# Kernel optimization log

Measured on AMD Instinct MI355X. Metric: run time of the kernel, lower is better.

## Reference

```python
import jax, jax.numpy as jnp
import numpy as np

DIM = 1024
NUM_HEADS = 16
HEAD_DIM = DIM // NUM_HEADS
EPS_NORM = 1e-12  # F.normalize eps
EPS_LN = 1e-5     # nn.LayerNorm eps


def setup_inputs() -> dict:
    key = jax.random.key(0)
    ks = jax.random.split(key, 6)
    x = jax.random.normal(ks[0], (4, 2048, DIM), dtype=jnp.float32)
    # LayerNorm params
    ln_w = jnp.ones((DIM,), jnp.float32)
    ln_b = jnp.zeros((DIM,), jnp.float32)
    # qkv: xavier_uniform on weight [3D, D], zero bias
    limit = float(np.sqrt(6.0 / (DIM + 3 * DIM)))
    qkv_w = jax.random.uniform(ks[1], (3 * DIM, DIM), jnp.float32, -limit, limit)
    qkv_b = jnp.zeros((3 * DIM,), jnp.float32)
    # out_proj: normal std=0.02, zero bias
    out_w = 0.02 * jax.random.normal(ks[2], (DIM, DIM), dtype=jnp.float32)
    out_b = jnp.zeros((DIM,), jnp.float32)
    return {"x": x, "ln_w": ln_w, "ln_b": ln_b, "qkv_w": qkv_w,
            "qkv_b": qkv_b, "out_w": out_w, "out_b": out_b}


def reference(x, ln_w, ln_b, qkv_w, qkv_b, out_w, out_b):
    B, N, D = x.shape
    # pre-LayerNorm
    mu = jnp.mean(x, axis=-1, keepdims=True)
    var = jnp.mean(jnp.square(x - mu), axis=-1, keepdims=True)
    h = (x - mu) / jnp.sqrt(var + EPS_LN) * ln_w + ln_b
    # QKV projection (torch Linear: y = h @ W^T + b)
    qkv = h @ qkv_w.T + qkv_b                     # [B, N, 3D]
    qkv = qkv.reshape(B, N, 3, NUM_HEADS, HEAD_DIM)
    q, k, v = (jnp.transpose(qkv[:, :, i], (0, 2, 1, 3)) for i in range(3))  # [B,H,N,hd]
    # per-head L2 normalize (F.normalize semantics: x / max(||x||, eps))
    q = q / jnp.maximum(jnp.linalg.norm(q, axis=-1, keepdims=True), EPS_NORM)
    k = k / jnp.maximum(jnp.linalg.norm(k, axis=-1, keepdims=True), EPS_NORM)
    scale = HEAD_DIM ** 0.5
    attn = jnp.einsum('bhqd,bhkd->bhqk', q, k) * scale
    attn = jax.nn.softmax(attn, axis=-1)
    out = jnp.einsum('bhqk,bhkd->bhqd', attn, v)  # [B,H,N,hd]
    out = jnp.transpose(out, (0, 2, 1, 3)).reshape(B, N, D)
    return x + out @ out_w.T + out_b
```

## Files before the change

### kernel.cpp

```cpp
#include <hip/hip_runtime.h>
#include <math.h>

constexpr int D     = 1024;
constexpr int NH    = 16;
constexpr int HD    = 64;
constexpr int SEQ   = 2048;
constexpr int BATCH = 4;
constexpr int NTOK  = BATCH * SEQ;

typedef short s16x8 __attribute__((ext_vector_type(8)));
typedef short s16x4 __attribute__((ext_vector_type(4)));
typedef float f32x4 __attribute__((ext_vector_type(4)));
typedef unsigned short u16;
typedef unsigned int   u32;

#if __has_builtin(__builtin_amdgcn_exp2f)
#define EXP2(x) __builtin_amdgcn_exp2f(x)
#else
#define EXP2(x) exp2f(x)
#endif

__device__ __forceinline__ short f2bf(float f) {
    unsigned u = __float_as_uint(f);
    unsigned r = (u + 0x7FFFu + ((u >> 16) & 1u)) >> 16;
    return (short)r;
}
__device__ __forceinline__ float bf2f(u16 s) {
    return __uint_as_float(((unsigned)s) << 16);
}

__device__ __forceinline__ u32 pack_bf16_pair(float f0, float f1) {
    u32 a = __float_as_uint(f1) + 0x8000u;
    u32 b = __float_as_uint(f0) + 0x8000u;
    return __builtin_amdgcn_perm(a, b, 0x07060302u);
}

__device__ __forceinline__ void async_lds16(const void* g, void* l) {
    __builtin_amdgcn_global_load_lds(
        (const __attribute__((address_space(1))) unsigned int*)g,
        (__attribute__((address_space(3))) unsigned int*)l, 16, 0, 0);
}

__device__ __forceinline__ float block_reduce_sum(float v, float* red) {
    int lane = threadIdx.x & 63, wid = threadIdx.x >> 6;
    #pragma unroll
    for (int off = 32; off > 0; off >>= 1) v += __shfl_down(v, off, 64);
    if (lane == 0) red[wid] = v;
    __syncthreads();
    float r = red[0] + red[1] + red[2] + red[3];
    __syncthreads();
    return r;
}

__global__ __launch_bounds__(256) void ln_kernel(const float* __restrict__ x,
                                                 const float* __restrict__ w,
                                                 const float* __restrict__ b,
                                                 u16* __restrict__ h) {
    __shared__ float red[4];
    int row = blockIdx.x;
    const float* xr = x + (size_t)row * D;
    int t = threadIdx.x;
    float v[4];
    float s = 0.f;
    #pragma unroll
    for (int i = 0; i < 4; i++) { v[i] = xr[t + 256 * i]; s += v[i]; }
    float mean = block_reduce_sum(s, red) * (1.0f / 1024.0f);
    float ss = 0.f;
    #pragma unroll
    for (int i = 0; i < 4; i++) { float d = v[i] - mean; ss += d * d; }
    float var = block_reduce_sum(ss, red) * (1.0f / 1024.0f);
    float rstd = rsqrtf(var + 1e-5f);
    u16* hr = h + (size_t)row * D;
    #pragma unroll
    for (int i = 0; i < 4; i++) {
        int c = t + 256 * i;
        hr[c] = (u16)f2bf((v[i] - mean) * rstd * w[c] + b[c]);
    }
}

__global__ __launch_bounds__(256) void cast_kernel(const float* __restrict__ in,
                                                   u16* __restrict__ out, int n) {
    int i = (blockIdx.x * 256 + threadIdx.x) * 4;
    if (i >= n) return;
    float4 f = *(const float4*)(in + i);
    s16x4 o4;
    o4[0] = f2bf(f.x); o4[1] = f2bf(f.y); o4[2] = f2bf(f.z); o4[3] = f2bf(f.w);
    *(s16x4*)(out + i) = o4;
}

template <typename OutT, bool RES, bool NORMK>
__global__ __launch_bounds__(256) void gemm_bf16(const u16* __restrict__ A,
                                                 const u16* __restrict__ B,
                                                 const float* __restrict__ bias,
                                                 const float* __restrict__ R,
                                                 OutT* __restrict__ C,
                                                 int M, int N, int K) {
    __shared__ u16 As[128 * 32];
    __shared__ u16 Bs[128 * 32];
    int tid = threadIdx.x, wave = tid >> 6, lane = tid & 63;
    int quad = lane >> 4, l16 = lane & 15;
    int wm = (wave & 1) * 64, wn = (wave >> 1) * 64;
    int rowBase = blockIdx.y * 128, colBase = blockIdx.x * 128;

    int srow = lane >> 2;
    int sk8  = (lane & 3) * 8;

    f32x4 acc[4][4];
    #pragma unroll
    for (int i = 0; i < 4; i++)
        #pragma unroll
        for (int j = 0; j < 4; j++)
            acc[i][j] = (f32x4){0.f, 0.f, 0.f, 0.f};

    for (int k0 = 0; k0 < K; k0 += 32) {
        __syncthreads();
        #pragma unroll
        for (int i = 0; i < 2; i++) {
            int r = wave * 32 + i * 16;
            const u16* ga = A + (size_t)(rowBase + r + srow) * K + k0 + sk8;
            async_lds16(ga, &As[r * 32]);
            const u16* gb = B + (size_t)(colBase + r + srow) * K + k0 + sk8;
            async_lds16(gb, &Bs[r * 32]);
        }
        __syncthreads();

        s16x8 af[4], bfr[4];
        #pragma unroll
        for (int t = 0; t < 4; t++) {
            af[t]  = *(const s16x8*)&As[(wm + t * 16 + l16) * 32 + quad * 8];
            bfr[t] = *(const s16x8*)&Bs[(wn + t * 16 + l16) * 32 + quad * 8];
        }
        #pragma unroll
        for (int mt = 0; mt < 4; mt++)
            #pragma unroll
            for (int nt = 0; nt < 4; nt++)
                acc[mt][nt] = __builtin_amdgcn_mfma_f32_16x16x32_bf16(
                    af[mt], bfr[nt], acc[mt][nt], 0, 0, 0);
    }

    bool normk = NORMK && (colBase + wn) >= 1024 && (colBase + wn) < 2048;

    #pragma unroll
    for (int mt = 0; mt < 4; mt++) {
        float vals[4][4];
        #pragma unroll
        for (int nt = 0; nt < 4; nt++) {
            int gn = colBase + wn + nt * 16 + l16;
            float bv = bias[gn];
            #pragma unroll
            for (int r = 0; r < 4; r++) {
                float val = acc[mt][nt][r] + bv;
                if (RES) {
                    int gm = rowBase + wm + mt * 16 + quad * 4 + r;
                    val += R[(size_t)gm * N + gn];
                }
                vals[nt][r] = val;
            }
        }
        if (normk) {
            #pragma unroll
            for (int r = 0; r < 4; r++) {
                float ssq = 0.f;
                #pragma unroll
                for (int nt = 0; nt < 4; nt++) ssq = fmaf(vals[nt][r], vals[nt][r], ssq);
                ssq += __shfl_xor(ssq, 1, 64);
                ssq += __shfl_xor(ssq, 2, 64);
                ssq += __shfl_xor(ssq, 4, 64);
                ssq += __shfl_xor(ssq, 8, 64);
                float inv = 1.0f / fmaxf(sqrtf(ssq), 1e-12f);
                #pragma unroll
                for (int nt = 0; nt < 4; nt++) vals[nt][r] *= inv;
            }
        }
        #pragma unroll
        for (int nt = 0; nt < 4; nt++) {
            int gn = colBase + wn + nt * 16 + l16;
            int gm0 = rowBase + wm + mt * 16 + quad * 4;
            #pragma unroll
            for (int r = 0; r < 4; r++) {
                if constexpr (sizeof(OutT) == 2)
                    C[(size_t)(gm0 + r) * N + gn] = (OutT)f2bf(vals[nt][r]);
                else
                    C[(size_t)(gm0 + r) * N + gn] = vals[nt][r];
            }
        }
    }
}

__device__ __forceinline__ s16x8 rdfrag(const u16* lds, int row, int kk, int quad) {
    int byte = row * 128 + ((kk * 64 + quad * 16) ^ ((row & 7) << 4));
    return *(const s16x8*)((const char*)lds + byte);
}

__device__ __forceinline__ void stage_half_A(const u16* __restrict__ A, u16* ldsA,
                                             int rowBase, int K, int kt, int hs,
                                             int wave, int lane) {
    #pragma unroll
    for (int i = 0; i < 2; i++) {
        int c = wave * 2 + i;
        int baserow = ((c & 7) * 8) + ((c >> 3) << 7) + (hs << 6);
        int row = baserow + (lane >> 3);
        int colb = ((lane & 7) * 16) ^ ((row & 7) << 4);
        const u16* src = A + (size_t)(rowBase + row) * K + kt * 64 + (colb >> 1);
        async_lds16(src, ldsA + baserow * 64);
    }
}
__device__ __forceinline__ void stage_half_B(const u16* __restrict__ B, u16* ldsB,
                                             int colBase, int K, int kt, int hs,
                                             int wave, int lane) {
    #pragma unroll
    for (int i = 0; i < 2; i++) {
        int c = wave * 2 + i;
        int baserow = ((c & 3) * 8) + ((c >> 2) << 6) + (hs << 5);
        int row = baserow + (lane >> 3);
        int colb = ((lane & 7) * 16) ^ ((row & 7) << 4);
        const u16* src = B + (size_t)(colBase + row) * K + kt * 64 + (colb >> 1);
        async_lds16(src, ldsB + baserow * 64);
    }
}

template <typename OutT, bool RES, bool NORMK>
__global__ __launch_bounds__(512, 2) void gemm256(const u16* __restrict__ A,
                                                  const u16* __restrict__ B,
                                                  const float* __restrict__ bias,
                                                  const float* __restrict__ R,
                                                  OutT* __restrict__ C,
                                                  int M, int N, int K) {
    __shared__ u16 lds[2][2][256 * 64];

    int nby = M >> 8;
    int cpx = gridDim.x >> 3;
    int bid = blockIdx.x;
    int swz = (bid & 7) * cpx + (bid >> 3);
    int bx = swz / nby, by = swz % nby;
    int rowBase = by << 8, colBase = bx << 8;

    int tid = threadIdx.x, wave = tid >> 6, lane = tid & 63;
    int quad = lane >> 4, l16 = lane & 15;
    int wr = wave >> 2, wc = wave & 3;
    int KT = K >> 6;

    f32x4 acc[8][4];
    #pragma unroll
    for (int m = 0; m < 8; m++)
        #pragma unroll
        for (int n = 0; n < 4; n++)
            acc[m][n] = (f32x4){0.f, 0.f, 0.f, 0.f};

    stage_half_A(A, &lds[0][0][0], rowBase, K, 0, 0, wave, lane);
    stage_half_B(B, &lds[0][1][0], colBase, K, 0, 0, wave, lane);
    stage_half_A(A, &lds[0][0][0], rowBase, K, 0, 1, wave, lane);
    stage_half_B(B, &lds[0][1][0], colBase, K, 0, 1, wave, lane);
    stage_half_A(A, &lds[1][0][0], rowBase, K, 1, 0, wave, lane);
    stage_half_B(B, &lds[1][1][0], colBase, K, 1, 0, wave, lane);
    stage_half_A(A, &lds[1][0][0], rowBase, K, 1, 1, wave, lane);
    asm volatile("s_waitcnt vmcnt(6)" ::: "memory");
    __builtin_amdgcn_s_barrier();

    for (int t = 0; t < KT; ++t) {
        int bsel = t & 1;
        u16* cA = &lds[bsel][0][0];
        u16* cB = &lds[bsel][1][0];
        u16* oB = &lds[bsel ^ 1][1][0];
        int t1 = t + 1; if (t1 >= KT) t1 -= KT;
        int t2 = t + 2; if (t2 >= KT) t2 -= KT;

        s16x8 af[4][2], bf0[2][2], bf1[2][2];

        #pragma unroll
        for (int m = 0; m < 4; m++)
            #pragma unroll
            for (int kk = 0; kk < 2; kk++)
                af[m][kk] = rdfrag(cA, wr * 128 + m * 16 + l16, kk, quad);
        #pragma unroll
        for (int n = 0; n < 2; n++)
            #pragma unroll
            for (int kk = 0; kk < 2; kk++)
                bf0[n][kk] = rdfrag(cB, wc * 64 + n * 16 + l16, kk, quad);
        stage_half_B(B, oB, colBase, K, t1, 1, wave, lane);
        __builtin_amdgcn_s_barrier();
        __builtin_amdgcn_s_setprio(1);
        #pragma unroll
        for (int kk = 0; kk < 2; kk++)
            #pragma unroll
            for (int m = 0; m < 4; m++)
                #pragma unroll
                for (int n = 0; n < 2; n++)
                    acc[m][n] = __builtin_amdgcn_mfma_f32_16x16x32_bf16(
                        af[m][kk], bf0[n][kk], acc[m][n], 0, 0, 0);
        __builtin_amdgcn_s_setprio(0);
        __builtin_amdgcn_s_barrier();

        #pragma unroll
        for (int n = 0; n < 2; n++)
            #pragma unroll
            for (int kk = 0; kk < 2; kk++)
                bf1[n][kk] = rdfrag(cB, wc * 64 + (n + 2) * 16 + l16, kk, quad);
        stage_half_A(A, cA, rowBase, K, t2, 0, wave, lane);
        __builtin_amdgcn_s_barrier();
        __builtin_amdgcn_s_setprio(1);
        #pragma unroll
        for (int kk = 0; kk < 2; kk++)
            #pragma unroll
            for (int m = 0; m < 4; m++)
                #pragma unroll
                for (int n = 0; n < 2; n++)
                    acc[m][n + 2] = __builtin_amdgcn_mfma_f32_16x16x32_bf16(
                        af[m][kk], bf1[n][kk], acc[m][n + 2], 0, 0, 0);
        __builtin_amdgcn_s_setprio(0);
        __builtin_amdgcn_s_barrier();

        #pragma unroll
        for (int m = 0; m < 4; m++)
            #pragma unroll
            for (int kk = 0; kk < 2; kk++)
                af[m][kk] = rdfrag(cA, wr * 128 + (m + 4) * 16 + l16, kk, quad);
        stage_half_B(B, cB, colBase, K, t2, 0, wave, lane);
        __builtin_amdgcn_s_barrier();
        __builtin_amdgcn_s_setprio(1);
        #pragma unroll
        for (int kk = 0; kk < 2; kk++)
            #pragma unroll
            for (int m = 0; m < 4; m++)
                #pragma unroll
                for (int n = 0; n < 2; n++)
                    acc[m + 4][n] = __builtin_amdgcn_mfma_f32_16x16x32_bf16(
                        af[m][kk], bf0[n][kk], acc[m + 4][n], 0, 0, 0);
        __builtin_amdgcn_s_setprio(0);
        __builtin_amdgcn_s_barrier();

        stage_half_A(A, cA, rowBase, K, t2, 1, wave, lane);
        __builtin_amdgcn_s_barrier();
        __builtin_amdgcn_s_setprio(1);
        #pragma unroll
        for (int kk = 0; kk < 2; kk++)
            #pragma unroll
            for (int m = 0; m < 4; m++)
                #pragma unroll
                for (int n = 0; n < 2; n++)
                    acc[m + 4][n + 2] = __builtin_amdgcn_mfma_f32_16x16x32_bf16(
                        af[m][kk], bf1[n][kk], acc[m + 4][n + 2], 0, 0, 0);
        __builtin_amdgcn_s_setprio(0);
        asm volatile("s_waitcnt vmcnt(6)" ::: "memory");
        __builtin_amdgcn_s_barrier();
    }
    asm volatile("s_waitcnt vmcnt(0)" ::: "memory");

    bool normk = NORMK && (colBase + wc * 64) >= 1024 && (colBase + wc * 64) < 2048;

    #pragma unroll
    for (int m = 0; m < 8; m++) {
        float vals[4][4];
        #pragma unroll
        for (int n = 0; n < 4; n++) {
            int gn = colBase + wc * 64 + n * 16 + l16;
            float bv = bias[gn];
            #pragma unroll
            for (int r = 0; r < 4; r++) {
                float val = acc[m][n][r] + bv;
                if (RES) {
                    int gm = rowBase + wr * 128 + m * 16 + quad * 4 + r;
                    val += R[(size_t)gm * N + gn];
                }
                vals[n][r] = val;
            }
        }
        if (normk) {
            #pragma unroll
            for (int r = 0; r < 4; r++) {
                float ssq = 0.f;
                #pragma unroll
                for (int n = 0; n < 4; n++) ssq = fmaf(vals[n][r], vals[n][r], ssq);
                ssq += __shfl_xor(ssq, 1, 64);
                ssq += __shfl_xor(ssq, 2, 64);
                ssq += __shfl_xor(ssq, 4, 64);
                ssq += __shfl_xor(ssq, 8, 64);
                float inv = 1.0f / fmaxf(sqrtf(ssq), 1e-12f);
                #pragma unroll
                for (int n = 0; n < 4; n++) vals[n][r] *= inv;
            }
        }
        #pragma unroll
        for (int n = 0; n < 4; n++) {
            int gn = colBase + wc * 64 + n * 16 + l16;
            int gm0 = rowBase + wr * 128 + m * 16 + quad * 4;
            #pragma unroll
            for (int r = 0; r < 4; r++) {
                if constexpr (sizeof(OutT) == 2)
                    C[(size_t)(gm0 + r) * N + gn] = (OutT)f2bf(vals[n][r]);
                else
                    C[(size_t)(gm0 + r) * N + gn] = vals[n][r];
            }
        }
    }
}

__global__ __launch_bounds__(256, 2) void mha_kernel(const u16* __restrict__ qkv,
                                                     u16* __restrict__ out) {
    __shared__ u16 Ks[64 * 64];
    constexpr int VS = 68;
    __shared__ u16 Vt[64 * VS];

    int bh = blockIdx.x & 63;
    int qt = blockIdx.x >> 6;
    int b  = bh >> 4, h = bh & 15;
    int tid = threadIdx.x;
    int wave = tid >> 6, lane = tid & 63;
    int quad = lane >> 4, l16 = lane & 15;

    const size_t rs = 3072;
    constexpr float SCL = 11.5415605f;

    s16x8 aq[4][2];
    #pragma unroll
    for (int rt = 0; rt < 4; rt++) {
        const u16* qb = qkv + ((size_t)(b * SEQ) + qt * 256 + wave * 64 + rt * 16 + l16) * rs + h * 64;
        s16x8 r0 = *(const s16x8*)(qb + quad * 8);
        s16x8 r1 = *(const s16x8*)(qb + 32 + quad * 8);
        float f0[8], f1[8], ss = 0.f;
        #pragma unroll
        for (int i = 0; i < 8; i++) { f0[i] = bf2f((u16)r0[i]); ss = fmaf(f0[i], f0[i], ss); }
        #pragma unroll
        for (int i = 0; i < 8; i++) { f1[i] = bf2f((u16)r1[i]); ss = fmaf(f1[i], f1[i], ss); }
        ss += __shfl_xor(ss, 16, 64);
        ss += __shfl_xor(ss, 32, 64);
        float inv = SCL / fmaxf(sqrtf(ss), 1e-12f);
        #pragma unroll
        for (int i = 0; i < 8; i++) {
            aq[rt][0][i] = f2bf(f0[i] * inv);
            aq[rt][1][i] = f2bf(f1[i] * inv);
        }
    }

    const f32x4 cinit = {-SCL, -SCL, -SCL, -SCL};
    f32x4 o2[4][4];
    f32x4 osum[4];
    #pragma unroll
    for (int rt = 0; rt < 4; rt++) {
        #pragma unroll
        for (int ht = 0; ht < 4; ht++) o2[rt][ht] = (f32x4){0.f, 0.f, 0.f, 0.f};
        osum[rt] = (f32x4){0.f, 0.f, 0.f, 0.f};
    }
    s16x8 ones;
    #pragma unroll
    for (int i = 0; i < 8; i++) ones[i] = (short)0x3F80;

    int skey = tid >> 2, c4 = tid & 3;
    int ksw  = skey & 7;
    int vp2 = tid >> 3, dc = (tid & 7) * 8;
    const u16* kglob  = qkv + ((size_t)(b * SEQ) + skey) * rs + 1024 + h * 64 + c4 * 16;
    const u16* vglob0 = qkv + ((size_t)(b * SEQ) + 2 * vp2) * rs + 2048 + h * 64 + dc;
    u16* kdst0 = &Ks[skey * 64 + ((2 * c4)     ^ ksw) * 8];
    u16* kdst1 = &Ks[skey * 64 + ((2 * c4 + 1) ^ ksw) * 8];
    u32* vt32 = (u32*)&Vt[0];

    s16x8 kr0 = ((const s16x8*)kglob)[0];
    s16x8 kr1 = ((const s16x8*)kglob)[1];
    s16x8 vr0 = *(const s16x8*)(vglob0);
    s16x8 vr1 = *(const s16x8*)(vglob0 + rs);

    int swz = l16 & 7;

    for (int kb = 0; kb < SEQ / 64; kb++) {
        __syncthreads();
        *(s16x8*)kdst0 = kr0;
        *(s16x8*)kdst1 = kr1;
        #pragma unroll
        for (int i = 0; i < 8; i++) {
            u32 pk = (u32)(u16)vr0[i] | ((u32)(u16)vr1[i] << 16);
            vt32[(dc + i) * (VS / 2) + vp2] = pk;
        }
        __syncthreads();

        if (kb < SEQ / 64 - 1) {
            const u16* kp = kglob + (size_t)(kb + 1) * 64 * rs;
            const u16* vp = vglob0 + (size_t)(kb + 1) * 64 * rs;
            kr0 = ((const s16x8*)kp)[0];
            kr1 = ((const s16x8*)kp)[1];
            vr0 = *(const s16x8*)(vp);
            vr1 = *(const s16x8*)(vp + rs);
        }

        s16x4 pfr[4][4];
        #pragma unroll
        for (int t = 0; t < 4; t++) {
            const u16* krow = &Ks[(t * 16 + l16) * 64];
            s16x8 bk0 = *(const s16x8*)(krow + ((0 + quad) ^ swz) * 8);
            s16x8 bk1 = *(const s16x8*)(krow + ((4 + quad) ^ swz) * 8);
            #pragma unroll
            for (int rt = 0; rt < 4; rt++) {
                f32x4 s = cinit;
                s = __builtin_amdgcn_mfma_f32_16x16x32_bf16(bk0, aq[rt][0], s, 0, 0, 0);
                s = __builtin_amdgcn_mfma_f32_16x16x32_bf16(bk1, aq[rt][1], s, 0, 0, 0);
                uint2 pk2;
                pk2.x = pack_bf16_pair(EXP2(s[0]), EXP2(s[1]));
                pk2.y = pack_bf16_pair(EXP2(s[2]), EXP2(s[3]));
                pfr[rt][t] = __builtin_bit_cast(s16x4, pk2);
            }
        }

        #pragma unroll
        for (int pr = 0; pr < 2; pr++) {
            int tA = pr * 2, tB = pr * 2 + 1;
            s16x8 bp[4];
            #pragma unroll
            for (int rt = 0; rt < 4; rt++)
                bp[rt] = __builtin_shufflevector(pfr[rt][tA], pfr[rt][tB],
                                                 0, 1, 2, 3, 4, 5, 6, 7);
            #pragma unroll
            for (int ht = 0; ht < 4; ht++) {
                const u16* vrow = &Vt[(ht * 16 + l16) * VS];
                s16x4 va = *(const s16x4*)(vrow + tA * 16 + quad * 4);
                s16x4 vb = *(const s16x4*)(vrow + tB * 16 + quad * 4);
                s16x8 vfr = __builtin_shufflevector(va, vb, 0, 1, 2, 3, 4, 5, 6, 7);
                #pragma unroll
                for (int rt = 0; rt < 4; rt++)
                    o2[rt][ht] = __builtin_amdgcn_mfma_f32_16x16x32_bf16(
                        vfr, bp[rt], o2[rt][ht], 0, 0, 0);
            }
            #pragma unroll
            for (int rt = 0; rt < 4; rt++)
                osum[rt] = __builtin_amdgcn_mfma_f32_16x16x32_bf16(
                    ones, bp[rt], osum[rt], 0, 0, 0);
        }
    }

    #pragma unroll
    for (int rt = 0; rt < 4; rt++) {
        float inv = 1.0f / osum[rt][0];
        int orow = b * SEQ + qt * 256 + wave * 64 + rt * 16 + l16;
        u16* op = out + (size_t)orow * D + h * 64 + quad * 4;
        #pragma unroll
        for (int ht = 0; ht < 4; ht++) {
            f32x4 v = o2[rt][ht];
            u32 lo = pack_bf16_pair(v[0] * inv, v[1] * inv);
            u32 hi = pack_bf16_pair(v[2] * inv, v[3] * inv);
            uint2 pk = {lo, hi};
            *(uint2*)(op + ht * 16) = pk;
        }
    }
}

extern "C" void kernel_launch(void* const* d_in, const int* in_sizes, int n_in,
                              void* d_out, int out_size, void* d_ws, size_t ws_size,
                              hipStream_t stream) {
    const float* x     = (const float*)d_in[0];
    const float* ln_w  = (const float*)d_in[1];
    const float* ln_b  = (const float*)d_in[2];
    const float* qkv_w = (const float*)d_in[3];
    const float* qkv_b = (const float*)d_in[4];
    const float* out_w = (const float*)d_in[5];
    const float* out_b = (const float*)d_in[6];
    float* y = (float*)d_out;

    char* ws = (char*)d_ws;
    u16* qkv = (u16*)ws;
    u16* h   = (u16*)(ws + (size_t)48 * 1024 * 1024);
    u16* wq  = (u16*)(ws + (size_t)64 * 1024 * 1024);
    u16* wo  = (u16*)(ws + (size_t)70 * 1024 * 1024);
    u16* attn_out = h;

    ln_kernel<<<NTOK, 256, 0, stream>>>(x, ln_w, ln_b, h);
    cast_kernel<<<(3 * D * D) / 1024, 256, 0, stream>>>(qkv_w, wq, 3 * D * D);
    cast_kernel<<<(D * D) / 1024, 256, 0, stream>>>(out_w, wo, D * D);

    {
        dim3 grid(3 * D / 128, NTOK / 128);
        gemm_bf16<u16, false, true><<<grid, 256, 0, stream>>>(h, wq, qkv_b, nullptr,
                                                              qkv, NTOK, 3 * D, D);
    }

    mha_kernel<<<BATCH * NH * (SEQ / 256), 256, 0, stream>>>(qkv, attn_out);

    gemm256<float, true, false><<<(D / 256) * (NTOK / 256), 512, 0, stream>>>(
        attn_out, wo, out_b, x, y, NTOK, D, D);
}
```

Before: 295.6 us.

## Use 8 waves per attention block and merge LN with weight casts

The attention kernel now launches 512 threads per block, each wave handling 32 query rows instead of 64. This halves per-wave accumulator registers and raises the launch-bound occupancy target, and only the first 256 threads stage K/V into LDS. Separately, the LayerNorm and the two weight-cast kernels are merged into one launch to save launch overhead. The trade-off is that each wave gets less K/V reuse per LDS load, and half the threads idle during staging.

```diff
diff --git a/kernel.cpp b/kernel.cpp
--- a/kernel.cpp
+++ b/kernel.cpp
@@ -52,40 +52,48 @@
     return r;
 }
 
-__global__ __launch_bounds__(256) void ln_kernel(const float* __restrict__ x,
-                                                 const float* __restrict__ w,
-                                                 const float* __restrict__ b,
-                                                 u16* __restrict__ h) {
+__global__ __launch_bounds__(256) void prep_kernel(const float* __restrict__ x,
+                                                   const float* __restrict__ w,
+                                                   const float* __restrict__ b,
+                                                   u16* __restrict__ h,
+                                                   const float* __restrict__ wq_in,
+                                                   u16* __restrict__ wq_out,
+                                                   const float* __restrict__ wo_in,
+                                                   u16* __restrict__ wo_out) {
     __shared__ float red[4];
-    int row = blockIdx.x;
-    const float* xr = x + (size_t)row * D;
+    int blk = blockIdx.x;
     int t = threadIdx.x;
-    float v[4];
-    float s = 0.f;
-    #pragma unroll
-    for (int i = 0; i < 4; i++) { v[i] = xr[t + 256 * i]; s += v[i]; }
-    float mean = block_reduce_sum(s, red) * (1.0f / 1024.0f);
-    float ss = 0.f;
-    #pragma unroll
-    for (int i = 0; i < 4; i++) { float d = v[i] - mean; ss += d * d; }
-    float var = block_reduce_sum(ss, red) * (1.0f / 1024.0f);
-    float rstd = rsqrtf(var + 1e-5f);
-    u16* hr = h + (size_t)row * D;
-    #pragma unroll
-    for (int i = 0; i < 4; i++) {
-        int c = t + 256 * i;
-        hr[c] = (u16)f2bf((v[i] - mean) * rstd * w[c] + b[c]);
-    }
-}
-
-__global__ __launch_bounds__(256) void cast_kernel(const float* __restrict__ in,
-                                                   u16* __restrict__ out, int n) {
-    int i = (blockIdx.x * 256 + threadIdx.x) * 4;
-    if (i >= n) return;
-    float4 f = *(const float4*)(in + i);
-    s16x4 o4;
-    o4[0] = f2bf(f.x); o4[1] = f2bf(f.y); o4[2] = f2bf(f.z); o4[3] = f2bf(f.w);
-    *(s16x4*)(out + i) = o4;
+    if (blk < NTOK) {
+        const float* xr = x + (size_t)blk * D;
+        float v[4];
+        float s = 0.f;
+        #pragma unroll
+        for (int i = 0; i < 4; i++) { v[i] = xr[t + 256 * i]; s += v[i]; }
+        float mean = block_reduce_sum(s, red) * (1.0f / 1024.0f);
+        float ss = 0.f;
+        #pragma unroll
+        for (int i = 0; i < 4; i++) { float d = v[i] - mean; ss += d * d; }
+        float var = block_reduce_sum(ss, red) * (1.0f / 1024.0f);
+        float rstd = rsqrtf(var + 1e-5f);
+        u16* hr = h + (size_t)blk * D;
+        #pragma unroll
+        for (int i = 0; i < 4; i++) {
+            int c = t + 256 * i;
+            hr[c] = (u16)f2bf((v[i] - mean) * rstd * w[c] + b[c]);
+        }
+    } else if (blk < NTOK + 3072) {
+        int i = ((blk - NTOK) * 256 + t) * 4;
+        float4 f = *(const float4*)(wq_in + i);
+        s16x4 o4;
+        o4[0] = f2bf(f.x); o4[1] = f2bf(f.y); o4[2] = f2bf(f.z); o4[3] = f2bf(f.w);
+        *(s16x4*)(wq_out + i) = o4;
+    } else {
+        int i = ((blk - NTOK - 3072) * 256 + t) * 4;
+        float4 f = *(const float4*)(wo_in + i);
+        s16x4 o4;
+        o4[0] = f2bf(f.x); o4[1] = f2bf(f.y); o4[2] = f2bf(f.z); o4[3] = f2bf(f.w);
+        *(s16x4*)(wo_out + i) = o4;
+    }
 }
 
 template <typename OutT, bool RES, bool NORMK>
@@ -395,7 +403,7 @@
     }
 }
 
-__global__ __launch_bounds__(256, 2) void mha_kernel(const u16* __restrict__ qkv,
+__global__ __launch_bounds__(512, 4) void mha_kernel(const u16* __restrict__ qkv,
                                                      u16* __restrict__ out) {
     __shared__ u16 Ks[64 * 64];
     constexpr int VS = 68;
@@ -411,10 +419,10 @@
     const size_t rs = 3072;
     constexpr float SCL = 11.5415605f;
 
-    s16x8 aq[4][2];
-    #pragma unroll
-    for (int rt = 0; rt < 4; rt++) {
-        const u16* qb = qkv + ((size_t)(b * SEQ) + qt * 256 + wave * 64 + rt * 16 + l16) * rs + h * 64;
+    s16x8 aq[2][2];
+    #pragma unroll
+    for (int rt = 0; rt < 2; rt++) {
+        const u16* qb = qkv + ((size_t)(b * SEQ) + qt * 256 + wave * 32 + rt * 16 + l16) * rs + h * 64;
         s16x8 r0 = *(const s16x8*)(qb + quad * 8);
         s16x8 r1 = *(const s16x8*)(qb + 32 + quad * 8);
         float f0[8], f1[8], ss = 0.f;
@@ -433,10 +441,10 @@
     }
 
     const f32x4 cinit = {-SCL, -SCL, -SCL, -SCL};
-    f32x4 o2[4][4];
-    f32x4 osum[4];
-    #pragma unroll
-    for (int rt = 0; rt < 4; rt++) {
+    f32x4 o2[2][4];
+    f32x4 osum[2];
+    #pragma unroll
+    for (int rt = 0; rt < 2; rt++) {
         #pragma unroll
         for (int ht = 0; ht < 4; ht++) o2[rt][ht] = (f32x4){0.f, 0.f, 0.f, 0.f};
         osum[rt] = (f32x4){0.f, 0.f, 0.f, 0.f};
@@ -445,34 +453,41 @@
     #pragma unroll
     for (int i = 0; i < 8; i++) ones[i] = (short)0x3F80;
 
-    int skey = tid >> 2, c4 = tid & 3;
+    bool stager = (tid < 256);
+    int st = tid & 255;
+    int skey = st >> 2, c4 = st & 3;
     int ksw  = skey & 7;
-    int vp2 = tid >> 3, dc = (tid & 7) * 8;
+    int vp2 = st >> 3, dc = (st & 7) * 8;
     const u16* kglob  = qkv + ((size_t)(b * SEQ) + skey) * rs + 1024 + h * 64 + c4 * 16;
     const u16* vglob0 = qkv + ((size_t)(b * SEQ) + 2 * vp2) * rs + 2048 + h * 64 + dc;
     u16* kdst0 = &Ks[skey * 64 + ((2 * c4)     ^ ksw) * 8];
     u16* kdst1 = &Ks[skey * 64 + ((2 * c4 + 1) ^ ksw) * 8];
     u32* vt32 = (u32*)&Vt[0];
 
-    s16x8 kr0 = ((const s16x8*)kglob)[0];
-    s16x8 kr1 = ((const s16x8*)kglob)[1];
-    s16x8 vr0 = *(const s16x8*)(vglob0);
-    s16x8 vr1 = *(const s16x8*)(vglob0 + rs);
+    s16x8 kr0{}, kr1{}, vr0{}, vr1{};
+    if (stager) {
+        kr0 = ((const s16x8*)kglob)[0];
+        kr1 = ((const s16x8*)kglob)[1];
+        vr0 = *(const s16x8*)(vglob0);
+        vr1 = *(const s16x8*)(vglob0 + rs);
+    }
 
     int swz = l16 & 7;
 
     for (int kb = 0; kb < SEQ / 64; kb++) {
         __syncthreads();
-        *(s16x8*)kdst0 = kr0;
-        *(s16x8*)kdst1 = kr1;
-        #pragma unroll
-        for (int i = 0; i < 8; i++) {
-            u32 pk = (u32)(u16)vr0[i] | ((u32)(u16)vr1[i] << 16);
-            vt32[(dc + i) * (VS / 2) + vp2] = pk;
+        if (stager) {
+            *(s16x8*)kdst0 = kr0;
+            *(s16x8*)kdst1 = kr1;
+            #pragma unroll
+            for (int i = 0; i < 8; i++) {
+                u32 pk = (u32)(u16)vr0[i] | ((u32)(u16)vr1[i] << 16);
+                vt32[(dc + i) * (VS / 2) + vp2] = pk;
+            }
         }
         __syncthreads();
 
-        if (kb < SEQ / 64 - 1) {
+        if (stager && kb < SEQ / 64 - 1) {
             const u16* kp = kglob + (size_t)(kb + 1) * 64 * rs;
             const u16* vp = vglob0 + (size_t)(kb + 1) * 64 * rs;
             kr0 = ((const s16x8*)kp)[0];
@@ -481,14 +496,14 @@
             vr1 = *(const s16x8*)(vp + rs);
         }
 
-        s16x4 pfr[4][4];
+        s16x4 pfr[2][4];
         #pragma unroll
         for (int t = 0; t < 4; t++) {
             const u16* krow = &Ks[(t * 16 + l16) * 64];
             s16x8 bk0 = *(const s16x8*)(krow + ((0 + quad) ^ swz) * 8);
             s16x8 bk1 = *(const s16x8*)(krow + ((4 + quad) ^ swz) * 8);
             #pragma unroll
-            for (int rt = 0; rt < 4; rt++) {
+            for (int rt = 0; rt < 2; rt++) {
                 f32x4 s = cinit;
                 s = __builtin_amdgcn_mfma_f32_16x16x32_bf16(bk0, aq[rt][0], s, 0, 0, 0);
                 s = __builtin_amdgcn_mfma_f32_16x16x32_bf16(bk1, aq[rt][1], s, 0, 0, 0);
@@ -502,9 +517,9 @@
         #pragma unroll
         for (int pr = 0; pr < 2; pr++) {
             int tA = pr * 2, tB = pr * 2 + 1;
-            s16x8 bp[4];
-            #pragma unroll
-            for (int rt = 0; rt < 4; rt++)
+            s16x8 bp[2];
+            #pragma unroll
+            for (int rt = 0; rt < 2; rt++)
                 bp[rt] = __builtin_shufflevector(pfr[rt][tA], pfr[rt][tB],
                                                  0, 1, 2, 3, 4, 5, 6, 7);
             #pragma unroll
@@ -514,21 +529,21 @@
                 s16x4 vb = *(const s16x4*)(vrow + tB * 16 + quad * 4);
                 s16x8 vfr = __builtin_shufflevector(va, vb, 0, 1, 2, 3, 4, 5, 6, 7);
                 #pragma unroll
-                for (int rt = 0; rt < 4; rt++)
+                for (int rt = 0; rt < 2; rt++)
                     o2[rt][ht] = __builtin_amdgcn_mfma_f32_16x16x32_bf16(
                         vfr, bp[rt], o2[rt][ht], 0, 0, 0);
             }
             #pragma unroll
-            for (int rt = 0; rt < 4; rt++)
+            for (int rt = 0; rt < 2; rt++)
                 osum[rt] = __builtin_amdgcn_mfma_f32_16x16x32_bf16(
                     ones, bp[rt], osum[rt], 0, 0, 0);
         }
     }
 
     #pragma unroll
-    for (int rt = 0; rt < 4; rt++) {
+    for (int rt = 0; rt < 2; rt++) {
         float inv = 1.0f / osum[rt][0];
-        int orow = b * SEQ + qt * 256 + wave * 64 + rt * 16 + l16;
+        int orow = b * SEQ + qt * 256 + wave * 32 + rt * 16 + l16;
         u16* op = out + (size_t)orow * D + h * 64 + quad * 4;
         #pragma unroll
         for (int ht = 0; ht < 4; ht++) {
@@ -560,9 +575,8 @@
     u16* wo  = (u16*)(ws + (size_t)70 * 1024 * 1024);
     u16* attn_out = h;
 
-    ln_kernel<<<NTOK, 256, 0, stream>>>(x, ln_w, ln_b, h);
-    cast_kernel<<<(3 * D * D) / 1024, 256, 0, stream>>>(qkv_w, wq, 3 * D * D);
-    cast_kernel<<<(D * D) / 1024, 256, 0, stream>>>(out_w, wo, D * D);
+    prep_kernel<<<NTOK + 3072 + 1024, 256, 0, stream>>>(x, ln_w, ln_b, h,
+                                                        qkv_w, wq, out_w, wo);
 
     {
         dim3 grid(3 * D / 128, NTOK / 128);
@@ -570,7 +584,7 @@
                                                               qkv, NTOK, 3 * D, D);
     }
 
-    mha_kernel<<<BATCH * NH * (SEQ / 256), 256, 0, stream>>>(qkv, attn_out);
+    mha_kernel<<<BATCH * NH * (SEQ / 256), 512, 0, stream>>>(qkv, attn_out);
 
     gemm256<float, true, false><<<(D / 256) * (NTOK / 256), 512, 0, stream>>>(
         attn_out, wo, out_b, x, y, NTOK, D, D);
```

New measurement: 289.3 us. -2.1%, faster.
